# Kernel optimization log

Measured on AMD Instinct MI355X. Metric: run time of the kernel, lower is better.

## Reference

```python
import jax, jax.numpy as jnp
import numpy as np

B, T, D, VQ, L2, HID = 8, 2048, 768, 64, 12, 1024
K = 2 ** L2          # 4096 codebook entries
N_MID = 4            # condition_layer=6 -> 1 input + 4 middle + 1 output Linear, 5 BatchNorms
EPS_N = 1e-6
EPS_BN = 1e-5


def setup_inputs() -> dict:
    key = jax.random.key(0)
    ks = jax.random.split(key, 10)
    g = lambda i, shape, sc: jax.random.normal(ks[i], shape, jnp.float32) * sc
    return {
        "h_in": jax.random.normal(ks[0], (B, D, T), jnp.float32),
        "attn_mask": jax.random.randint(ks[1], (B, T), 0, 2, jnp.int32),
        "proj_w": g(2, (VQ, D), 0.02), "proj_b": jnp.zeros((VQ,), jnp.float32),
        "inv_w": g(3, (D, VQ), 0.02), "inv_b": jnp.zeros((D,), jnp.float32),
        "mlp_w_in": g(4, (HID, L2), 0.1), "mlp_b_in": jnp.zeros((HID,), jnp.float32),
        "mlp_w_mid": g(5, (N_MID, HID, HID), 0.03), "mlp_b_mid": jnp.zeros((N_MID, HID), jnp.float32),
        "mlp_w_out": g(6, (VQ, HID), 0.03), "mlp_b_out": jnp.zeros((VQ,), jnp.float32),
        "bn_gamma": jnp.ones((N_MID + 1, HID), jnp.float32),
        "bn_beta": jnp.zeros((N_MID + 1, HID), jnp.float32),
    }


def _bn(x, gamma, beta):
    # BatchNorm1d, training mode: batch mean / biased var over codebook rows
    m = x.mean(axis=0)
    v = x.var(axis=0)
    return (x - m) * jax.lax.rsqrt(v + EPS_BN) * gamma + beta


def _l2norm(x):
    return x / (jnp.linalg.norm(x, axis=-1, keepdims=True) + EPS_N)


def reference(h_in, attn_mask, proj_w, proj_b, inv_w, inv_b,
              mlp_w_in, mlp_b_in, mlp_w_mid, mlp_b_mid, mlp_w_out, mlp_b_out,
              bn_gamma, bn_beta):
    # --- codebook: binary vectors -> condition MLP (Linear+BN+ReLU x5, Linear) ---
    ints = jnp.arange(K)
    bits = ((ints[:, None] & (1 << jnp.arange(L2 - 1, -1, -1))) > 0).astype(jnp.float32)  # [K, L2]
    x = jax.nn.relu(_bn(bits @ mlp_w_in.T + mlp_b_in, bn_gamma[0], bn_beta[0]))
    for i in range(N_MID):
        x = jax.nn.relu(_bn(x @ mlp_w_mid[i].T + mlp_b_mid[i], bn_gamma[i + 1], bn_beta[i + 1]))
    embed = x @ mlp_w_out.T + mlp_b_out          # [K, VQ]
    embed = _l2norm(embed)                        # sphere=True

    # --- project hidden states: h_in [B,D,T] -> [B,T,VQ] ---
    h = jnp.einsum('bdt,vd->btv', h_in, proj_w) + proj_b
    h = _l2norm(h)

    # --- pairwise squared distances to codebook, argmax of -d (== softmax argmax) ---
    hf = h.reshape(-1, VQ)                                       # [B*T, VQ]
    d = (hf ** 2).sum(-1, keepdims=True) + (embed ** 2).sum(-1) - 2.0 * (hf @ embed.T)  # [B*T, K]
    code = jnp.argmax(-d, axis=-1)                               # [B*T]

    # --- masked gather/scatter quantization (eval path: hard codes) ---
    mask = (attn_mask == 1)                                      # [B, T]
    h_vq = embed[code].reshape(B, T, VQ) * mask[..., None].astype(h.dtype)
    quantized = jnp.einsum('btv,dv->btd', h_vq, inv_w) + inv_b   # proj_inv -> [B, T, D]
    vq_code = jnp.where(mask, code.reshape(B, T), 0)
    return quantized, vq_code
```

## Files before the change

kernel.cpp:

```cpp
#include <hip/hip_runtime.h>
#include <stddef.h>

#define BB   8
#define TT_  2048
#define DD   768
#define VQ_  64
#define L2C  12
#define HID_ 1024
#define KK   4096
#define NMID 4
#define NT   (BB*TT_)

typedef _Float16 h8v __attribute__((ext_vector_type(8)));
typedef float    f4v __attribute__((ext_vector_type(4)));

#define GL16(g, l) __builtin_amdgcn_global_load_lds( \
    (const __attribute__((address_space(1))) void*)(g), \
    (__attribute__((address_space(3))) void*)(l), 16, 0, 0)

__global__ __launch_bounds__(256) void k_mlp_in(const float* __restrict__ w_in,
                                                const float* __restrict__ b_in,
                                                float* __restrict__ X) {
    __shared__ float ws_[256 * 12];
    __shared__ float bs_[256];
    int tid = threadIdx.x;
    int h0  = blockIdx.x * 256;
    for (int i = tid; i < 256 * 12; i += 256) ws_[i] = w_in[h0 * 12 + i];
    bs_[tid] = b_in[h0 + tid];
    __syncthreads();
    float w[12];
#pragma unroll
    for (int l = 0; l < 12; l++) w[l] = ws_[tid * 12 + l];
    float bias = bs_[tid];
    int k0 = blockIdx.y * 16;
    for (int kk = 0; kk < 16; kk++) {
        int k = k0 + kk;
        float acc = bias;
#pragma unroll
        for (int l = 0; l < 12; l++)
            if ((k >> (11 - l)) & 1) acc += w[l];
        X[(size_t)k * HID_ + h0 + tid] = acc;
    }
}

__global__ __launch_bounds__(256) void k_bn_stats1(const float* __restrict__ Y,
                                                   float* __restrict__ part) {
    int b = blockIdx.x;
    int c = blockIdx.y * 256 + threadIdx.x;
    const float* src = Y + ((size_t)b << 6) * HID_ + c;
    float s = 0.f, q = 0.f;
    for (int r = 0; r < 64; r++) {
        float v = src[(size_t)r << 10];
        s += v; q += v * v;
    }
    part[((size_t)b << 10) + c] = s;
    part[65536 + ((size_t)b << 10) + c] = q;
}

__global__ __launch_bounds__(256) void k_bn_stats2(const float* __restrict__ part,
                                                   float* __restrict__ mv) {
    int c = blockIdx.x * 256 + threadIdx.x;
    float s = 0.f, q = 0.f;
    for (int b = 0; b < 64; b++) {
        s += part[((size_t)b << 10) + c];
        q += part[65536 + ((size_t)b << 10) + c];
    }
    float m = s * (1.f / KK);
    float v = q * (1.f / KK) - m * m;
    mv[c] = m; mv[HID_ + c] = v;
}

__global__ __launch_bounds__(256) void k_bn_apply_split(const float* __restrict__ Y,
                                                        const float* __restrict__ mv,
                                                        const float* __restrict__ gamma,
                                                        const float* __restrict__ beta,
                                                        _Float16* __restrict__ Xhi,
                                                        _Float16* __restrict__ Xlo) {
    int i = blockIdx.x * 256 + threadIdx.x;
    int c = (i << 2) & (HID_ - 1);
    float4 x = ((const float4*)Y)[i];
    float4 m = *(const float4*)(mv + c);
    float4 v = *(const float4*)(mv + HID_ + c);
    float4 g = *(const float4*)(gamma + c);
    float4 b = *(const float4*)(beta + c);
    float o[4];
    o[0] = fmaxf(0.f, (x.x - m.x) * (1.f / sqrtf(v.x + 1e-5f)) * g.x + b.x);
    o[1] = fmaxf(0.f, (x.y - m.y) * (1.f / sqrtf(v.y + 1e-5f)) * g.y + b.y);
    o[2] = fmaxf(0.f, (x.z - m.z) * (1.f / sqrtf(v.z + 1e-5f)) * g.z + b.z);
    o[3] = fmaxf(0.f, (x.w - m.w) * (1.f / sqrtf(v.w + 1e-5f)) * g.w + b.w);
    union { _Float16 h[4]; uint2 u; } uh, ul;
#pragma unroll
    for (int j = 0; j < 4; j++) {
        _Float16 h = (_Float16)o[j];
        uh.h[j] = h;
        ul.h[j] = (_Float16)(o[j] - (float)h);
    }
    *(uint2*)(Xhi + ((size_t)i << 2)) = uh.u;
    *(uint2*)(Xlo + ((size_t)i << 2)) = ul.u;
}

__global__ __launch_bounds__(256) void k_gemm_mfma3(const _Float16* __restrict__ Ahi,
                                                    const _Float16* __restrict__ Alo,
                                                    const _Float16* __restrict__ Whi,
                                                    const _Float16* __restrict__ Wlo,
                                                    const float* __restrict__ bias,
                                                    float* __restrict__ C) {
    __shared__ __attribute__((aligned(128))) char lds[4 * 32768];
    const int tid = threadIdx.x;
    const int wg = blockIdx.x;
    const int m0 = (wg & 31) << 7;
    const int n0 = (wg >> 5) << 7;
    const int wave = tid >> 6, lane = tid & 63;
    const int l15 = lane & 15, quad = lane >> 4;
    const int wm = (wave >> 1) << 6;
    const int wn = (wave & 1) << 6;

    const int rowA = (wave << 5) + (lane >> 2);
    const int colb = (lane & 3) << 4;
    const char* gA_h = (const char*)Ahi + ((size_t)(m0 + rowA) << 11) + colb;
    const char* gA_l = (const char*)Alo + ((size_t)(m0 + rowA) << 11) + colb;
    const char* gW_h = (const char*)Whi + ((size_t)(n0 + rowA) << 11) + colb;
    const char* gW_l = (const char*)Wlo + ((size_t)(n0 + rowA) << 11) + colb;
    const int dA = wave << 11;

    int offA[4], offW[4];
#pragma unroll
    for (int i = 0; i < 4; i++) offA[i] = ((wm + (i << 4) + l15) << 6) + (quad << 4);
#pragma unroll
    for (int j = 0; j < 4; j++) offW[j] = ((wn + (j << 4) + l15) << 6) + (quad << 4);

    f4v acc[4][4];
#pragma unroll
    for (int i = 0; i < 4; i++)
#pragma unroll
        for (int j = 0; j < 4; j++) acc[i][j] = (f4v){0.f, 0.f, 0.f, 0.f};

#define STG(bufi, tt) do { \
        char* b_ = lds + ((bufi) << 15); int o_ = (tt) << 6; \
        GL16(gA_h + o_,         b_ + dA); \
        GL16(gA_h + 32768 + o_, b_ + dA + 1024); \
        GL16(gA_l + o_,         b_ + 8192 + dA); \
        GL16(gA_l + 32768 + o_, b_ + 8192 + dA + 1024); \
        GL16(gW_h + o_,         b_ + 16384 + dA); \
        GL16(gW_h + 32768 + o_, b_ + 16384 + dA + 1024); \
        GL16(gW_l + o_,         b_ + 24576 + dA); \
        GL16(gW_l + 32768 + o_, b_ + 24576 + dA + 1024); \
    } while (0)

    STG(0, 0); STG(1, 1); STG(2, 2);
    for (int t = 0; t < 32; ++t) {
        if (t <= 29)      asm volatile("s_waitcnt vmcnt(16)" ::: "memory");
        else if (t == 30) asm volatile("s_waitcnt vmcnt(8)"  ::: "memory");
        else              asm volatile("s_waitcnt vmcnt(0)"  ::: "memory");
        __builtin_amdgcn_s_barrier();
        asm volatile("" ::: "memory");
        if (t + 3 < 32) STG((t + 3) & 3, t + 3);
        const char* b = lds + ((size_t)(t & 3) << 15);
        h8v ah[4], al[4];
#pragma unroll
        for (int i = 0; i < 4; i++) {
            ah[i] = *(const h8v*)(b + offA[i]);
            al[i] = *(const h8v*)(b + 8192 + offA[i]);
        }
        __builtin_amdgcn_s_setprio(1);
#pragma unroll
        for (int j = 0; j < 4; j++) {
            h8v bh = *(const h8v*)(b + 16384 + offW[j]);
            h8v bl = *(const h8v*)(b + 24576 + offW[j]);
#pragma unroll
            for (int i = 0; i < 4; i++) {
                acc[i][j] = __builtin_amdgcn_mfma_f32_16x16x32_f16(ah[i], bh, acc[i][j], 0, 0, 0);
                acc[i][j] = __builtin_amdgcn_mfma_f32_16x16x32_f16(ah[i], bl, acc[i][j], 0, 0, 0);
                acc[i][j] = __builtin_amdgcn_mfma_f32_16x16x32_f16(al[i], bh, acc[i][j], 0, 0, 0);
            }
        }
        __builtin_amdgcn_s_setprio(0);
        asm volatile("" ::: "memory");
    }
#undef STG

#pragma unroll
    for (int j = 0; j < 4; j++) {
        int col = n0 + wn + (j << 4) + l15;
        float bv = bias[col];
#pragma unroll
        for (int i = 0; i < 4; i++) {
            int row = m0 + wm + (i << 4) + (quad << 2);
#pragma unroll
            for (int r = 0; r < 4; r++)
                C[(size_t)(row + r) * HID_ + col] = acc[i][j][r] + bv;
        }
    }
}

__global__ __launch_bounds__(256) void k_gemm_mfma2(const _Float16* __restrict__ Ahi,
                                                    const _Float16* __restrict__ Alo,
                                                    const _Float16* __restrict__ Whi,
                                                    const _Float16* __restrict__ Wlo,
                                                    const float* __restrict__ bias,
                                                    float* __restrict__ C,
                                                    int M, int N, int Kd) {
    __shared__ __attribute__((aligned(128))) char lds[2][24576];
    const int tid = threadIdx.x;
    int wg = blockIdx.x;
    const int nwg = gridDim.x;
    wg = (wg & 7) * (nwg >> 3) + (wg >> 3);
    const int nx = M >> 7;
    const int m0 = (wg % nx) << 7;
    const int n0 = (wg / nx) << 6;
    const int wave = tid >> 6, lane = tid & 63;
    const int l15 = lane & 15, quad = lane >> 4;
    const int wm = (wave >> 1) << 6;
    const int wn = (wave & 1) << 5;

    const int pA0 = ((wave << 1) | 0) * 1024 + lane * 16;
    const int pA1 = ((wave << 1) | 1) * 1024 + lane * 16;
    const int pW  = wave * 1024 + lane * 16;
    const int qA0 = pA0 ^ (((pA0 >> 7) & 3) << 4);
    const int qA1 = pA1 ^ (((pA1 >> 7) & 3) << 4);
    const int qW  = pW  ^ (((pW  >> 7) & 3) << 4);
    const size_t krow = (size_t)Kd * 2;
    const char* gAh0 = (const char*)Ahi + (size_t)(m0 + (qA0 >> 6)) * krow + (qA0 & 63);
    const char* gAh1 = (const char*)Ahi + (size_t)(m0 + (qA1 >> 6)) * krow + (qA1 & 63);
    const char* gAl0 = (const char*)Alo + (size_t)(m0 + (qA0 >> 6)) * krow + (qA0 & 63);
    const char* gAl1 = (const char*)Alo + (size_t)(m0 + (qA1 >> 6)) * krow + (qA1 & 63);
    const char* gWh  = (const char*)Whi + (size_t)(n0 + (qW >> 6)) * krow + (qW & 63);
    const char* gWl  = (const char*)Wlo + (size_t)(n0 + (qW >> 6)) * krow + (qW & 63);
    const int dA0 = (wave << 1) * 1024;
    const int dA1 = dA0 + 1024;
    const int dW  = wave * 1024;

    int offA[4], offW[2];
#pragma unroll
    for (int i = 0; i < 4; i++) {
        int r = wm + (i << 4) + l15;
        offA[i] = r * 64 + ((quad ^ ((r >> 1) & 3)) << 4);
    }
#pragma unroll
    for (int j = 0; j < 2; j++) {
        int r = wn + (j << 4) + l15;
        offW[j] = r * 64 + ((quad ^ ((r >> 1) & 3)) << 4);
    }

    f4v acc[4][2];
#pragma unroll
    for (int i = 0; i < 4; i++)
#pragma unroll
        for (int j = 0; j < 2; j++) acc[i][j] = (f4v){0.f, 0.f, 0.f, 0.f};

#define STAGE(bufi, tt) do { \
        char* b_ = lds[bufi]; size_t o_ = (size_t)(tt) << 6; \
        GL16(gAh0 + o_, b_ + dA0); \
        GL16(gAh1 + o_, b_ + dA1); \
        GL16(gAl0 + o_, b_ + 8192 + dA0); \
        GL16(gAl1 + o_, b_ + 8192 + dA1); \
        GL16(gWh  + o_, b_ + 16384 + dW); \
        GL16(gWl  + o_, b_ + 20480 + dW); \
    } while (0)

    STAGE(0, 0);
    const int nt = Kd >> 5;
    for (int t = 0; t < nt; ++t) {
        const int cur = t & 1;
        if (t + 1 < nt) {
            STAGE(cur ^ 1, t + 1);
            asm volatile("s_waitcnt vmcnt(6)" ::: "memory");
        } else {
            asm volatile("s_waitcnt vmcnt(0)" ::: "memory");
        }
        __builtin_amdgcn_s_barrier();
        asm volatile("" ::: "memory");
        const char* b = lds[cur];
        h8v ah[4], al[4], bh[2], bl[2];
#pragma unroll
        for (int i = 0; i < 4; i++) {
            ah[i] = *(const h8v*)(b + offA[i]);
            al[i] = *(const h8v*)(b + 8192 + offA[i]);
        }
#pragma unroll
        for (int j = 0; j < 2; j++) {
            bh[j] = *(const h8v*)(b + 16384 + offW[j]);
            bl[j] = *(const h8v*)(b + 20480 + offW[j]);
        }
        __builtin_amdgcn_s_setprio(1);
#pragma unroll
        for (int i = 0; i < 4; i++)
#pragma unroll
            for (int j = 0; j < 2; j++) {
                acc[i][j] = __builtin_amdgcn_mfma_f32_16x16x32_f16(ah[i], bh[j], acc[i][j], 0, 0, 0);
                acc[i][j] = __builtin_amdgcn_mfma_f32_16x16x32_f16(ah[i], bl[j], acc[i][j], 0, 0, 0);
                acc[i][j] = __builtin_amdgcn_mfma_f32_16x16x32_f16(al[i], bh[j], acc[i][j], 0, 0, 0);
            }
        __builtin_amdgcn_s_setprio(0);
        asm volatile("" ::: "memory");
        __builtin_amdgcn_s_barrier();
    }
#undef STAGE

#pragma unroll
    for (int j = 0; j < 2; j++) {
        int col = n0 + wn + (j << 4) + l15;
        float bv = bias[col];
#pragma unroll
        for (int i = 0; i < 4; i++) {
            int row = m0 + wm + (i << 4) + (quad << 2);
#pragma unroll
            for (int r = 0; r < 4; r++)
                C[(size_t)(row + r) * N + col] = acc[i][j][r] + bv;
        }
    }
}

__global__ __launch_bounds__(256) void k_l2norm(float* __restrict__ E,
                                                float* __restrict__ eqh,
                                                _Float16* __restrict__ Ehi,
                                                _Float16* __restrict__ Elo) {
    int tid = threadIdx.x;
    int row = blockIdx.x * 4 + (tid >> 6);
    int v = tid & 63;
    size_t off = ((size_t)row << 6) + v;
    float x = E[off];
    float ss = x * x;
#pragma unroll
    for (int o = 32; o; o >>= 1) ss += __shfl_xor(ss, o, 64);
    float inv = 1.f / (sqrtf(ss) + 1e-6f);
    float xn = x * inv;
    E[off] = xn;
    _Float16 hh = (_Float16)xn;
    Ehi[off] = hh;
    Elo[off] = (_Float16)(xn - (float)hh);
    if (v == 0) eqh[row] = -0.5f * (ss * inv * inv);
}

__global__ __launch_bounds__(256) void k_wsplit(const float* __restrict__ pw,
                                                _Float16* __restrict__ pwhi,
                                                _Float16* __restrict__ pwlo) {
    int i = blockIdx.x * 256 + threadIdx.x;
    float4 w = ((const float4*)pw)[i];
    float wf[4] = {w.x, w.y, w.z, w.w};
    union { _Float16 h[4]; uint2 u; } uh, ul;
#pragma unroll
    for (int j = 0; j < 4; j++) {
        _Float16 h = (_Float16)wf[j];
        uh.h[j] = h;
        ul.h[j] = (_Float16)(wf[j] - (float)h);
    }
    *(uint2*)(pwhi + ((size_t)i << 2)) = uh.u;
    *(uint2*)(pwlo + ((size_t)i << 2)) = ul.u;
}

__global__ __launch_bounds__(256) void k_cvt_inv(const float* __restrict__ iw,
                                                 _Float16* __restrict__ iwh) {
    int i = blockIdx.x * 256 + threadIdx.x;
    float4 w = ((const float4*)iw)[i];
    union { _Float16 h[4]; uint2 u; } uh;
    uh.h[0] = (_Float16)w.x; uh.h[1] = (_Float16)w.y;
    uh.h[2] = (_Float16)w.z; uh.h[3] = (_Float16)w.w;
    *(uint2*)(iwh + ((size_t)i << 2)) = uh.u;
}

__global__ __launch_bounds__(256) void k_proj_mfma(const float* __restrict__ h_in,
                                                   const _Float16* __restrict__ pwhi,
                                                   const _Float16* __restrict__ pwlo,
                                                   float* __restrict__ Hpart) {
    __shared__ float shA[128 * 33];
    const int tid = threadIdx.x;
    const int t0 = blockIdx.x * 128;
    const int ks = blockIdx.y;
    const int b = t0 >> 11;
    const int tloc0 = t0 & (TT_ - 1);
    const int wave = tid >> 6, lane = tid & 63;
    const int l15 = lane & 15, quad = lane >> 4;

    const int dl = tid >> 3;
    const int tg = (tid & 7) << 4;

    f4v acc[2][4];
#pragma unroll
    for (int i = 0; i < 2; i++)
#pragma unroll
        for (int j = 0; j < 4; j++) acc[i][j] = (f4v){0.f, 0.f, 0.f, 0.f};

    for (int kk = 0; kk < 6; kk++) {
        int dd0 = ks * 192 + kk * 32;
        const float* src = h_in + ((size_t)(b * DD + dd0 + dl) << 11) + tloc0 + tg;
        float4 g0 = *(const float4*)(src);
        float4 g1 = *(const float4*)(src + 4);
        float4 g2 = *(const float4*)(src + 8);
        float4 g3 = *(const float4*)(src + 12);
        __syncthreads();
        float gv[16] = {g0.x, g0.y, g0.z, g0.w, g1.x, g1.y, g1.z, g1.w,
                        g2.x, g2.y, g2.z, g2.w, g3.x, g3.y, g3.z, g3.w};
#pragma unroll
        for (int i = 0; i < 16; i++) shA[(tg + i) * 33 + dl] = gv[i];
        __syncthreads();

        h8v ah[2], al[2];
#pragma unroll
        for (int mt = 0; mt < 2; mt++) {
            const float* ap = &shA[((wave << 5) + (mt << 4) + l15) * 33 + (quad << 3)];
            float4 a0 = *(const float4*)(ap);
            float4 a1 = *(const float4*)(ap + 4);
            float av[8] = {a0.x, a0.y, a0.z, a0.w, a1.x, a1.y, a1.z, a1.w};
#pragma unroll
            for (int j = 0; j < 8; j++) {
                _Float16 h = (_Float16)av[j];
                ah[mt][j] = h;
                al[mt][j] = (_Float16)(av[j] - (float)h);
            }
        }
#pragma unroll
        for (int nt = 0; nt < 4; nt++) {
            size_t wb = (size_t)((nt << 4) + l15) * DD + dd0 + (quad << 3);
            h8v bh = *(const h8v*)(pwhi + wb);
            h8v bl = *(const h8v*)(pwlo + wb);
#pragma unroll
            for (int mt = 0; mt < 2; mt++) {
                acc[mt][nt] = __builtin_amdgcn_mfma_f32_16x16x32_f16(ah[mt], bh, acc[mt][nt], 0, 0, 0);
                acc[mt][nt] = __builtin_amdgcn_mfma_f32_16x16x32_f16(ah[mt], bl, acc[mt][nt], 0, 0, 0);
                acc[mt][nt] = __builtin_amdgcn_mfma_f32_16x16x32_f16(al[mt], bh, acc[mt][nt], 0, 0, 0);
            }
        }
    }
    float* dst = Hpart + ((size_t)ks << 20);
#pragma unroll
    for (int mt = 0; mt < 2; mt++) {
#pragma unroll
        for (int r = 0; r < 4; r++) {
            int t = t0 + (wave << 5) + (mt << 4) + (quad << 2) + r;
#pragma unroll
            for (int nt = 0; nt < 4; nt++)
                dst[((size_t)t << 6) + (nt << 4) + l15] = acc[mt][nt][r];
        }
    }
}

__global__ __launch_bounds__(256) void k_hnorm(const float* __restrict__ Hpart,
                                               const float* __restrict__ pb,
                                               _Float16* __restrict__ Hhi,
                                               _Float16* __restrict__ Hlo) {
    __shared__ float ssp[4][64];
    int tid = threadIdx.x;
    int tt = tid & 63, vg = tid >> 6;
    int t = blockIdx.x * 64 + tt;
    size_t base = ((size_t)t << 6) + (vg << 4);
    float o[16];
#pragma unroll
    for (int u = 0; u < 4; u++) {
        float4 p0 = *(const float4*)(Hpart + (0u << 20) + base + (u << 2));
        float4 p1 = *(const float4*)(Hpart + (1u << 20) + base + (u << 2));
        float4 p2 = *(const float4*)(Hpart + (2u << 20) + base + (u << 2));
        float4 p3 = *(const float4*)(Hpart + (3u << 20) + base + (u << 2));
        o[u * 4 + 0] = p0.x + p1.x + p2.x + p3.x;
        o[u * 4 + 1] = p0.y + p1.y + p2.y + p3.y;
        o[u * 4 + 2] = p0.z + p1.z + p2.z + p3.z;
        o[u * 4 + 3] = p0.w + p1.w + p2.w + p3.w;
    }
    float sp = 0.f;
#pragma unroll
    for (int j = 0; j < 16; j++) {
        o[j] += pb[(vg << 4) + j];
        sp = fmaf(o[j], o[j], sp);
    }
    ssp[vg][tt] = sp;
    __syncthreads();
    float ss = ssp[0][tt] + ssp[1][tt] + ssp[2][tt] + ssp[3][tt];
    float inv = 1.f / (sqrtf(ss) + 1e-6f);
    union { _Float16 h[8]; uint4 u; } uh0, uh1, ul0, ul1;
#pragma unroll
    for (int j = 0; j < 16; j++) {
        float xn = o[j] * inv;
        _Float16 hh = (_Float16)xn;
        _Float16 ll = (_Float16)(xn - (float)hh);
        if (j < 8) { uh0.h[j] = hh; ul0.h[j] = ll; }
        else       { uh1.h[j - 8] = hh; ul1.h[j - 8] = ll; }
    }
    *(uint4*)(Hhi + base)     = uh0.u;
    *(uint4*)(Hhi + base + 8) = uh1.u;
    *(uint4*)(Hlo + base)     = ul0.u;
    *(uint4*)(Hlo + base + 8) = ul1.u;
}

__global__ __launch_bounds__(256) void k_argmax_mfma(const _Float16* __restrict__ Hhi,
                                                     const _Float16* __restrict__ Hlo,
                                                     const _Float16* __restrict__ Ehi,
                                                     const _Float16* __restrict__ Elo,
                                                     const float* __restrict__ eqh,
                                                     float* __restrict__ ps,
                                                     int* __restrict__ pi) {
    int tid = threadIdx.x;
    int wave = tid >> 6, lane = tid & 63;
    int l15 = lane & 15, quad = lane >> 4;
    int t0 = blockIdx.x * 256 + wave * 64;
    int kh = blockIdx.y;
    const int kbase = kh << 8;

    h8v hh0[4], hh1[4], hl0[4], hl1[4];
#pragma unroll
    for (int s = 0; s < 4; s++) {
        size_t hb = (size_t)(t0 + (s << 4) + l15) * 64 + (quad << 3);
        hh0[s] = *(const h8v*)(Hhi + hb);
        hh1[s] = *(const h8v*)(Hhi + hb + 32);
        hl0[s] = *(const h8v*)(Hlo + hb);
        hl1[s] = *(const h8v*)(Hlo + hb + 32);
    }
    float best[4] = {-1e30f, -1e30f, -1e30f, -1e30f};
    int   idx[4]  = {0, 0, 0, 0};

    size_t eb = (size_t)(kbase + l15) * 64 + (quad << 3);
    h8v eh0 = *(const h8v*)(Ehi + eb);
    h8v eh1 = *(const h8v*)(Ehi + eb + 32);
    h8v el0 = *(const h8v*)(Elo + eb);
    h8v el1 = *(const h8v*)(Elo + eb + 32);
    float4 q4 = *(const float4*)(eqh + kbase + (quad << 2));

    for (int it = 0; it < 16; it++) {
        h8v ce0 = eh0, ce1 = eh1, cl0 = el0, cl1 = el1;
        float4 cq = q4;
        int k0 = kbase + (it << 4);
        int kn = k0 + 16;
        if (kn > KK - 16) kn = KK - 16;
        size_t ebn = (size_t)(kn + l15) * 64 + (quad << 3);
        eh0 = *(const h8v*)(Ehi + ebn);
        eh1 = *(const h8v*)(Ehi + ebn + 32);
        el0 = *(const h8v*)(Elo + ebn);
        el1 = *(const h8v*)(Elo + ebn + 32);
        q4 = *(const float4*)(eqh + kn + (quad << 2));

        f4v acc[4];
#pragma unroll
        for (int s = 0; s < 4; s++) acc[s] = (f4v){0.f, 0.f, 0.f, 0.f};
#pragma unroll
        for (int s = 0; s < 4; s++) acc[s] = __builtin_amdgcn_mfma_f32_16x16x32_f16(ce0, hh0[s], acc[s], 0, 0, 0);
#pragma unroll
        for (int s = 0; s < 4; s++) acc[s] = __builtin_amdgcn_mfma_f32_16x16x32_f16(ce1, hh1[s], acc[s], 0, 0, 0);
#pragma unroll
        for (int s = 0; s < 4; s++) acc[s] = __builtin_amdgcn_mfma_f32_16x16x32_f16(cl0, hh0[s], acc[s], 0, 0, 0);
#pragma unroll
        for (int s = 0; s < 4; s++) acc[s] = __builtin_amdgcn_mfma_f32_16x16x32_f16(cl1, hh1[s], acc[s], 0, 0, 0);
#pragma unroll
        for (int s = 0; s < 4; s++) acc[s] = __builtin_amdgcn_mfma_f32_16x16x32_f16(ce0, hl0[s], acc[s], 0, 0, 0);
#pragma unroll
        for (int s = 0; s < 4; s++) acc[s] = __builtin_amdgcn_mfma_f32_16x16x32_f16(ce1, hl1[s], acc[s], 0, 0, 0);
        float qv[4] = {cq.x, cq.y, cq.z, cq.w};
#pragma unroll
        for (int r = 0; r < 4; r++) {
            int k = k0 + (quad << 2) + r;
#pragma unroll
            for (int s = 0; s < 4; s++) {
                float sc = acc[s][r] + qv[r];
                if (sc > best[s]) { best[s] = sc; idx[s] = k; }
            }
        }
    }
#pragma unroll
    for (int m = 16; m <= 32; m <<= 1) {
#pragma unroll
        for (int s = 0; s < 4; s++) {
            float ob = __shfl_xor(best[s], m, 64);
            int   oi = __shfl_xor(idx[s], m, 64);
            if (ob > best[s] || (ob == best[s] && oi < idx[s])) { best[s] = ob; idx[s] = oi; }
        }
    }
    if (quad == 0) {
#pragma unroll
        for (int s = 0; s < 4; s++) {
            int t = t0 + (s << 4) + l15;
            ps[(size_t)t * 16 + kh] = best[s];
            pi[(size_t)t * 16 + kh] = idx[s];
        }
    }
}

__global__ __launch_bounds__(256) void k_merge(const float* __restrict__ ps,
                                               const int* __restrict__ pi,
                                               const int* __restrict__ mask,
                                               const _Float16* __restrict__ Ehi,
                                               _Float16* __restrict__ G16,
                                               float* __restrict__ outc) {
    __shared__ int codes[256];
    __shared__ int ms[256];
    int tid = threadIdx.x;
    int base = blockIdx.x << 8;
    int t = base + tid;
    float best = ps[(size_t)t * 16];
    int bi = pi[(size_t)t * 16];
#pragma unroll
    for (int s = 1; s < 16; s++) {
        float v = ps[(size_t)t * 16 + s];
        if (v > best) { best = v; bi = pi[(size_t)t * 16 + s]; }
    }
    int m = mask[t];
    codes[tid] = bi;
    ms[tid] = m;
    outc[t] = m ? (float)bi : 0.0f;
    __syncthreads();
    for (int i = tid; i < 256 * 8; i += 256) {
        int r = i >> 3, u = i & 7;
        uint4 e = ms[r] ? ((const uint4*)(Ehi + ((size_t)codes[r] << 6)))[u]
                        : make_uint4(0u, 0u, 0u, 0u);
        ((uint4*)(G16 + ((size_t)(base + r) << 6)))[u] = e;
    }
}

__global__ __launch_bounds__(256) void k_gemm_out(const _Float16* __restrict__ G16,
                                                  const _Float16* __restrict__ iwh,
                                                  const float* __restrict__ bias,
                                                  float* __restrict__ C) {
    const int tid = threadIdx.x;
    const int t0 = blockIdx.x * 128, n0 = blockIdx.y * 64;
    const int wave = tid >> 6, lane = tid & 63;
    const int l15 = lane & 15, quad = lane >> 4;

    f4v acc[2][4];
#pragma unroll
    for (int i = 0; i < 2; i++)
#pragma unroll
        for (int j = 0; j < 4; j++) acc[i][j] = (f4v){0.f, 0.f, 0.f, 0.f};

#pragma unroll
    for (int ks = 0; ks < 2; ks++) {
        int kk = (ks << 5) + (quad << 3);
        h8v a[2], b[4];
#pragma unroll
        for (int mt = 0; mt < 2; mt++)
            a[mt] = *(const h8v*)(G16 + (size_t)(t0 + (wave << 5) + (mt << 4) + l15) * 64 + kk);
#pragma unroll
        for (int nt = 0; nt < 4; nt++)
            b[nt] = *(const h8v*)(iwh + (size_t)(n0 + (nt << 4) + l15) * 64 + kk);
#pragma unroll
        for (int mt = 0; mt < 2; mt++)
#pragma unroll
            for (int nt = 0; nt < 4; nt++)
                acc[mt][nt] = __builtin_amdgcn_mfma_f32_16x16x32_f16(a[mt], b[nt], acc[mt][nt], 0, 0, 0);
    }
#pragma unroll
    for (int nt = 0; nt < 4; nt++) {
        int col = n0 + (nt << 4) + l15;
        float bv = bias[col];
#pragma unroll
        for (int mt = 0; mt < 2; mt++) {
            int row = t0 + (wave << 5) + (mt << 4) + (quad << 2);
#pragma unroll
            for (int r = 0; r < 4; r++)
                C[(size_t)(row + r) * DD + col] = acc[mt][nt][r] + bv;
        }
    }
}

extern "C" void kernel_launch(void* const* d_in, const int* in_sizes, int n_in,
                              void* d_out, int out_size, void* d_ws, size_t ws_size,
                              hipStream_t stream) {
    const float* h_in   = (const float*)d_in[0];
    const int*   amask  = (const int*)d_in[1];
    const float* proj_w = (const float*)d_in[2];
    const float* proj_b = (const float*)d_in[3];
    const float* inv_w  = (const float*)d_in[4];
    const float* inv_b  = (const float*)d_in[5];
    const float* w_in   = (const float*)d_in[6];
    const float* b_in   = (const float*)d_in[7];
    const float* w_mid  = (const float*)d_in[8];
    const float* b_mid  = (const float*)d_in[9];
    const float* w_out  = (const float*)d_in[10];
    const float* b_out  = (const float*)d_in[11];
    const float* gamma  = (const float*)d_in[12];
    const float* beta   = (const float*)d_in[13];

    float*     Y    = (float*)d_ws;
    _Float16*  Xhi  = (_Float16*)(Y + (size_t)KK * HID_);
    _Float16*  Xlo  = Xhi + (size_t)KK * HID_;
    float*     mv   = (float*)(Xlo + (size_t)KK * HID_);
    float*     Emb  = mv + 2 * HID_;
    float*     eqh  = Emb + (size_t)KK * VQ_;
    float*     spart= eqh + KK;
    _Float16*  pwhi = (_Float16*)(spart + 2 * 65536);
    _Float16*  pwlo = pwhi + (size_t)VQ_ * DD;
    float*    Hpart = Y;
    _Float16* H16hi = Xhi;
    _Float16* H16lo = H16hi + (size_t)NT * VQ_;
    _Float16* E16hi = H16lo + (size_t)NT * VQ_;
    _Float16* E16lo = E16hi + (size_t)KK * VQ_;
    float*    ps    = (float*)(E16lo + (size_t)KK * VQ_);
    int*      pidx  = (int*)(ps + (size_t)NT * 16);
    _Float16* G16   = (_Float16*)(pidx + (size_t)NT * 16);
    _Float16* iwh   = G16 + (size_t)NT * VQ_;

    float* out_q = (float*)d_out;
    float* out_c = out_q + (size_t)NT * DD;

    _Float16* Wmh = (_Float16*)d_out;
    _Float16* Wml = Wmh + (size_t)HID_ * HID_;
    _Float16* Woh = Wml + (size_t)HID_ * HID_;
    _Float16* Wol = Woh + (size_t)VQ_ * HID_;

    k_mlp_in<<<dim3(HID_ / 256, KK / 16), 256, 0, stream>>>(w_in, b_in, Y);
    k_bn_stats1<<<dim3(64, 4), 256, 0, stream>>>(Y, spart);
    k_bn_stats2<<<4, 256, 0, stream>>>(spart, mv);
    k_bn_apply_split<<<KK * HID_ / 1024, 256, 0, stream>>>(Y, mv, gamma, beta, Xhi, Xlo);
    for (int i = 0; i < NMID; i++) {
        k_wsplit<<<HID_ * HID_ / 1024, 256, 0, stream>>>(
            w_mid + (size_t)i * HID_ * HID_, Wmh, Wml);
        k_gemm_mfma3<<<(KK / 128) * (HID_ / 128), 256, 0, stream>>>(
            Xhi, Xlo, Wmh, Wml, b_mid + (size_t)i * HID_, Y);
        k_bn_stats1<<<dim3(64, 4), 256, 0, stream>>>(Y, spart);
        k_bn_stats2<<<4, 256, 0, stream>>>(spart, mv);
        k_bn_apply_split<<<KK * HID_ / 1024, 256, 0, stream>>>(Y, mv,
            gamma + (size_t)(i + 1) * HID_, beta + (size_t)(i + 1) * HID_, Xhi, Xlo);
    }
    k_wsplit<<<VQ_ * HID_ / 1024, 256, 0, stream>>>(w_out, Woh, Wol);
    k_gemm_mfma2<<<(KK / 128) * (VQ_ / 64), 256, 0, stream>>>(
        Xhi, Xlo, Woh, Wol, b_out, Emb, KK, VQ_, HID_);
    k_l2norm<<<KK / 4, 256, 0, stream>>>(Emb, eqh, E16hi, E16lo);

    k_wsplit<<<VQ_ * DD / 1024, 256, 0, stream>>>(proj_w, pwhi, pwlo);
    k_cvt_inv<<<VQ_ * DD / 1024, 256, 0, stream>>>(inv_w, iwh);
    k_proj_mfma<<<dim3(NT / 128, 4), 256, 0, stream>>>(h_in, pwhi, pwlo, Hpart);
    k_hnorm<<<NT / 64, 256, 0, stream>>>(Hpart, proj_b, H16hi, H16lo);
    k_argmax_mfma<<<dim3(NT / 256, 16), 256, 0, stream>>>(
        H16hi, H16lo, E16hi, E16lo, eqh, ps, pidx);
    k_merge<<<NT / 256, 256, 0, stream>>>(ps, pidx, amask, E16hi, G16, out_c);
    k_gemm_out<<<dim3(NT / 128, DD / 64), 256, 0, stream>>>(G16, iwh, inv_b, out_q);
}
```

Measured before the change: 473.5 us.

## Batch weight splits into one launch, restructure GEMM and argmax pipelines

All fp16 hi/lo weight splits (mid, out, proj) now run in a single kernel at the start instead of six separate launches, which removes launch overhead. The mfma3 GEMM main loop now issues stages two at a time with a full vmcnt(0) wait per pair instead of a rolling 3-deep prefetch, which trades finer-grained overlap for fewer barriers. The argmax kernel halves the tokens per wave, doubles the grid and double-buffers two codebook tiles with interleaved MFMA chains, aiming for more occupancy and latency hiding. Staging the weights for all mid layers at once uses more scratch space in the output buffer.

```diff
diff --git a/kernel.cpp b/kernel.cpp
--- a/kernel.cpp
+++ b/kernel.cpp
@@ -147,36 +147,40 @@
         GL16(gW_l + 32768 + o_, b_ + 24576 + dA + 1024); \
     } while (0)
 
-    STG(0, 0); STG(1, 1); STG(2, 2);
-    for (int t = 0; t < 32; ++t) {
-        if (t <= 29)      asm volatile("s_waitcnt vmcnt(16)" ::: "memory");
-        else if (t == 30) asm volatile("s_waitcnt vmcnt(8)"  ::: "memory");
-        else              asm volatile("s_waitcnt vmcnt(0)"  ::: "memory");
+#define CMP(tt) do { \
+        const char* b = lds + ((size_t)((tt) & 3) << 15); \
+        h8v ah[4], al[4]; \
+        _Pragma("unroll") \
+        for (int i = 0; i < 4; i++) { \
+            ah[i] = *(const h8v*)(b + offA[i]); \
+            al[i] = *(const h8v*)(b + 8192 + offA[i]); \
+        } \
+        __builtin_amdgcn_s_setprio(1); \
+        _Pragma("unroll") \
+        for (int j = 0; j < 4; j++) { \
+            h8v bh = *(const h8v*)(b + 16384 + offW[j]); \
+            h8v bl = *(const h8v*)(b + 24576 + offW[j]); \
+            _Pragma("unroll") \
+            for (int i = 0; i < 4; i++) { \
+                acc[i][j] = __builtin_amdgcn_mfma_f32_16x16x32_f16(ah[i], bh, acc[i][j], 0, 0, 0); \
+                acc[i][j] = __builtin_amdgcn_mfma_f32_16x16x32_f16(ah[i], bl, acc[i][j], 0, 0, 0); \
+                acc[i][j] = __builtin_amdgcn_mfma_f32_16x16x32_f16(al[i], bh, acc[i][j], 0, 0, 0); \
+            } \
+        } \
+        __builtin_amdgcn_s_setprio(0); \
+    } while (0)
+
+    STG(0, 0); STG(1, 1);
+    for (int p = 0; p < 16; ++p) {
+        asm volatile("s_waitcnt vmcnt(0)" ::: "memory");
         __builtin_amdgcn_s_barrier();
         asm volatile("" ::: "memory");
-        if (t + 3 < 32) STG((t + 3) & 3, t + 3);
-        const char* b = lds + ((size_t)(t & 3) << 15);
-        h8v ah[4], al[4];
-#pragma unroll
-        for (int i = 0; i < 4; i++) {
-            ah[i] = *(const h8v*)(b + offA[i]);
-            al[i] = *(const h8v*)(b + 8192 + offA[i]);
-        }
-        __builtin_amdgcn_s_setprio(1);
-#pragma unroll
-        for (int j = 0; j < 4; j++) {
-            h8v bh = *(const h8v*)(b + 16384 + offW[j]);
-            h8v bl = *(const h8v*)(b + 24576 + offW[j]);
-#pragma unroll
-            for (int i = 0; i < 4; i++) {
-                acc[i][j] = __builtin_amdgcn_mfma_f32_16x16x32_f16(ah[i], bh, acc[i][j], 0, 0, 0);
-                acc[i][j] = __builtin_amdgcn_mfma_f32_16x16x32_f16(ah[i], bl, acc[i][j], 0, 0, 0);
-                acc[i][j] = __builtin_amdgcn_mfma_f32_16x16x32_f16(al[i], bh, acc[i][j], 0, 0, 0);
-            }
-        }
-        __builtin_amdgcn_s_setprio(0);
+        if (p < 15) { STG((2 * p + 2) & 3, 2 * p + 2); STG((2 * p + 3) & 3, 2 * p + 3); }
+        CMP(2 * p);
+        CMP(2 * p + 1);
         asm volatile("" ::: "memory");
     }
+#undef CMP
 #undef STG
 
 #pragma unroll
@@ -332,11 +336,21 @@
     if (v == 0) eqh[row] = -0.5f * (ss * inv * inv);
 }
 
-__global__ __launch_bounds__(256) void k_wsplit(const float* __restrict__ pw,
-                                                _Float16* __restrict__ pwhi,
-                                                _Float16* __restrict__ pwlo) {
+__global__ __launch_bounds__(256) void k_wsplit_all(const float* __restrict__ w_mid,
+                                                    const float* __restrict__ w_out,
+                                                    const float* __restrict__ proj_w,
+                                                    _Float16* __restrict__ Wmh,
+                                                    _Float16* __restrict__ Wml,
+                                                    _Float16* __restrict__ Woh,
+                                                    _Float16* __restrict__ Wol,
+                                                    _Float16* __restrict__ pwhi,
+                                                    _Float16* __restrict__ pwlo) {
     int i = blockIdx.x * 256 + threadIdx.x;
-    float4 w = ((const float4*)pw)[i];
+    const float4* src; _Float16 *dh, *dl; int off;
+    if (i < 1048576)            { src = (const float4*)w_mid;  dh = Wmh;  dl = Wml;  off = i; }
+    else if (i < 1048576+16384) { src = (const float4*)w_out;  dh = Woh;  dl = Wol;  off = i - 1048576; }
+    else                        { src = (const float4*)proj_w; dh = pwhi; dl = pwlo; off = i - 1048576 - 16384; }
+    float4 w = src[off];
     float wf[4] = {w.x, w.y, w.z, w.w};
     union { _Float16 h[4]; uint2 u; } uh, ul;
 #pragma unroll
@@ -345,8 +359,8 @@
         uh.h[j] = h;
         ul.h[j] = (_Float16)(wf[j] - (float)h);
     }
-    *(uint2*)(pwhi + ((size_t)i << 2)) = uh.u;
-    *(uint2*)(pwlo + ((size_t)i << 2)) = ul.u;
+    *(uint2*)(dh + ((size_t)off << 2)) = uh.u;
+    *(uint2*)(dl + ((size_t)off << 2)) = ul.u;
 }
 
 __global__ __launch_bounds__(256) void k_cvt_inv(const float* __restrict__ iw,
@@ -491,72 +505,81 @@
     int tid = threadIdx.x;
     int wave = tid >> 6, lane = tid & 63;
     int l15 = lane & 15, quad = lane >> 4;
-    int t0 = blockIdx.x * 256 + wave * 64;
+    int t0 = blockIdx.x * 128 + wave * 32;
     int kh = blockIdx.y;
     const int kbase = kh << 8;
 
-    h8v hh0[4], hh1[4], hl0[4], hl1[4];
-#pragma unroll
-    for (int s = 0; s < 4; s++) {
+    h8v hh0[2], hh1[2], hl0[2], hl1[2];
+#pragma unroll
+    for (int s = 0; s < 2; s++) {
         size_t hb = (size_t)(t0 + (s << 4) + l15) * 64 + (quad << 3);
         hh0[s] = *(const h8v*)(Hhi + hb);
         hh1[s] = *(const h8v*)(Hhi + hb + 32);
         hl0[s] = *(const h8v*)(Hlo + hb);
         hl1[s] = *(const h8v*)(Hlo + hb + 32);
     }
-    float best[4] = {-1e30f, -1e30f, -1e30f, -1e30f};
-    int   idx[4]  = {0, 0, 0, 0};
-
-    size_t eb = (size_t)(kbase + l15) * 64 + (quad << 3);
-    h8v eh0 = *(const h8v*)(Ehi + eb);
-    h8v eh1 = *(const h8v*)(Ehi + eb + 32);
-    h8v el0 = *(const h8v*)(Elo + eb);
-    h8v el1 = *(const h8v*)(Elo + eb + 32);
-    float4 q4 = *(const float4*)(eqh + kbase + (quad << 2));
-
-    for (int it = 0; it < 16; it++) {
-        h8v ce0 = eh0, ce1 = eh1, cl0 = el0, cl1 = el1;
-        float4 cq = q4;
-        int k0 = kbase + (it << 4);
-        int kn = k0 + 16;
-        if (kn > KK - 16) kn = KK - 16;
-        size_t ebn = (size_t)(kn + l15) * 64 + (quad << 3);
-        eh0 = *(const h8v*)(Ehi + ebn);
-        eh1 = *(const h8v*)(Ehi + ebn + 32);
-        el0 = *(const h8v*)(Elo + ebn);
-        el1 = *(const h8v*)(Elo + ebn + 32);
-        q4 = *(const float4*)(eqh + kn + (quad << 2));
-
-        f4v acc[4];
-#pragma unroll
-        for (int s = 0; s < 4; s++) acc[s] = (f4v){0.f, 0.f, 0.f, 0.f};
-#pragma unroll
-        for (int s = 0; s < 4; s++) acc[s] = __builtin_amdgcn_mfma_f32_16x16x32_f16(ce0, hh0[s], acc[s], 0, 0, 0);
-#pragma unroll
-        for (int s = 0; s < 4; s++) acc[s] = __builtin_amdgcn_mfma_f32_16x16x32_f16(ce1, hh1[s], acc[s], 0, 0, 0);
-#pragma unroll
-        for (int s = 0; s < 4; s++) acc[s] = __builtin_amdgcn_mfma_f32_16x16x32_f16(cl0, hh0[s], acc[s], 0, 0, 0);
-#pragma unroll
-        for (int s = 0; s < 4; s++) acc[s] = __builtin_amdgcn_mfma_f32_16x16x32_f16(cl1, hh1[s], acc[s], 0, 0, 0);
-#pragma unroll
-        for (int s = 0; s < 4; s++) acc[s] = __builtin_amdgcn_mfma_f32_16x16x32_f16(ce0, hl0[s], acc[s], 0, 0, 0);
-#pragma unroll
-        for (int s = 0; s < 4; s++) acc[s] = __builtin_amdgcn_mfma_f32_16x16x32_f16(ce1, hl1[s], acc[s], 0, 0, 0);
-        float qv[4] = {cq.x, cq.y, cq.z, cq.w};
-#pragma unroll
-        for (int r = 0; r < 4; r++) {
-            int k = k0 + (quad << 2) + r;
-#pragma unroll
-            for (int s = 0; s < 4; s++) {
-                float sc = acc[s][r] + qv[r];
-                if (sc > best[s]) { best[s] = sc; idx[s] = k; }
-            }
-        }
-    }
+    float best[2] = {-1e30f, -1e30f};
+    int   idx[2]  = {0, 0};
+
+    size_t eb0 = (size_t)(kbase + l15) * 64 + (quad << 3);
+    h8v e0h0 = *(const h8v*)(Ehi + eb0);
+    h8v e0h1 = *(const h8v*)(Ehi + eb0 + 32);
+    h8v e0l0 = *(const h8v*)(Elo + eb0);
+    h8v e0l1 = *(const h8v*)(Elo + eb0 + 32);
+    float4 q0 = *(const float4*)(eqh + kbase + (quad << 2));
+    size_t eb1 = eb0 + 1024;
+    h8v e1h0 = *(const h8v*)(Ehi + eb1);
+    h8v e1h1 = *(const h8v*)(Ehi + eb1 + 32);
+    h8v e1l0 = *(const h8v*)(Elo + eb1);
+    h8v e1l1 = *(const h8v*)(Elo + eb1 + 32);
+    float4 q1 = *(const float4*)(eqh + kbase + 16 + (quad << 2));
+
+#define AHALF(EH0, EH1, EL0, EL1, QQ, IT) do { \
+        f4v acc0 = (f4v){0.f, 0.f, 0.f, 0.f}; \
+        f4v acc1 = (f4v){0.f, 0.f, 0.f, 0.f}; \
+        __builtin_amdgcn_s_setprio(1); \
+        acc0 = __builtin_amdgcn_mfma_f32_16x16x32_f16(EH0, hh0[0], acc0, 0, 0, 0); \
+        acc1 = __builtin_amdgcn_mfma_f32_16x16x32_f16(EH0, hh0[1], acc1, 0, 0, 0); \
+        acc0 = __builtin_amdgcn_mfma_f32_16x16x32_f16(EH1, hh1[0], acc0, 0, 0, 0); \
+        acc1 = __builtin_amdgcn_mfma_f32_16x16x32_f16(EH1, hh1[1], acc1, 0, 0, 0); \
+        acc0 = __builtin_amdgcn_mfma_f32_16x16x32_f16(EL0, hh0[0], acc0, 0, 0, 0); \
+        acc1 = __builtin_amdgcn_mfma_f32_16x16x32_f16(EL0, hh0[1], acc1, 0, 0, 0); \
+        acc0 = __builtin_amdgcn_mfma_f32_16x16x32_f16(EL1, hh1[0], acc0, 0, 0, 0); \
+        acc1 = __builtin_amdgcn_mfma_f32_16x16x32_f16(EL1, hh1[1], acc1, 0, 0, 0); \
+        acc0 = __builtin_amdgcn_mfma_f32_16x16x32_f16(EH0, hl0[0], acc0, 0, 0, 0); \
+        acc1 = __builtin_amdgcn_mfma_f32_16x16x32_f16(EH0, hl0[1], acc1, 0, 0, 0); \
+        acc0 = __builtin_amdgcn_mfma_f32_16x16x32_f16(EH1, hl1[0], acc0, 0, 0, 0); \
+        acc1 = __builtin_amdgcn_mfma_f32_16x16x32_f16(EH1, hl1[1], acc1, 0, 0, 0); \
+        __builtin_amdgcn_s_setprio(0); \
+        float cqa[4] = {QQ.x, QQ.y, QQ.z, QQ.w}; \
+        int tn = (IT) + 2; if (tn > 15) tn = 15;       \
+        size_t ebn = (size_t)(kbase + (tn << 4) + l15) * 64 + (quad << 3); \
+        EH0 = *(const h8v*)(Ehi + ebn); \
+        EH1 = *(const h8v*)(Ehi + ebn + 32); \
+        EL0 = *(const h8v*)(Elo + ebn); \
+        EL1 = *(const h8v*)(Elo + ebn + 32); \
+        QQ  = *(const float4*)(eqh + kbase + (tn << 4) + (quad << 2)); \
+        int k0 = kbase + ((IT) << 4); \
+        _Pragma("unroll") \
+        for (int r = 0; r < 4; r++) { \
+            int kk_ = k0 + (quad << 2) + r; \
+            float sc0 = acc0[r] + cqa[r]; \
+            if (sc0 > best[0]) { best[0] = sc0; idx[0] = kk_; } \
+            float sc1 = acc1[r] + cqa[r]; \
+            if (sc1 > best[1]) { best[1] = sc1; idx[1] = kk_; } \
+        } \
+    } while (0)
+
+    for (int p = 0; p < 8; ++p) {
+        AHALF(e0h0, e0h1, e0l0, e0l1, q0, 2 * p);
+        AHALF(e1h0, e1h1, e1l0, e1l1, q1, 2 * p + 1);
+    }
+#undef AHALF
+
 #pragma unroll
     for (int m = 16; m <= 32; m <<= 1) {
 #pragma unroll
-        for (int s = 0; s < 4; s++) {
+        for (int s = 0; s < 2; s++) {
             float ob = __shfl_xor(best[s], m, 64);
             int   oi = __shfl_xor(idx[s], m, 64);
             if (ob > best[s] || (ob == best[s] && oi < idx[s])) { best[s] = ob; idx[s] = oi; }
@@ -564,7 +587,7 @@
     }
     if (quad == 0) {
 #pragma unroll
-        for (int s = 0; s < 4; s++) {
+        for (int s = 0; s < 2; s++) {
             int t = t0 + (s << 4) + l15;
             ps[(size_t)t * 16 + kh] = best[s];
             pi[(size_t)t * 16 + kh] = idx[s];
@@ -689,34 +712,34 @@
     float* out_c = out_q + (size_t)NT * DD;
 
     _Float16* Wmh = (_Float16*)d_out;
-    _Float16* Wml = Wmh + (size_t)HID_ * HID_;
-    _Float16* Woh = Wml + (size_t)HID_ * HID_;
+    _Float16* Wml = Wmh + (size_t)NMID * HID_ * HID_;
+    _Float16* Woh = Wml + (size_t)NMID * HID_ * HID_;
     _Float16* Wol = Woh + (size_t)VQ_ * HID_;
+
+    k_wsplit_all<<<4208, 256, 0, stream>>>(w_mid, w_out, proj_w,
+                                           Wmh, Wml, Woh, Wol, pwhi, pwlo);
 
     k_mlp_in<<<dim3(HID_ / 256, KK / 16), 256, 0, stream>>>(w_in, b_in, Y);
     k_bn_stats1<<<dim3(64, 4), 256, 0, stream>>>(Y, spart);
     k_bn_stats2<<<4, 256, 0, stream>>>(spart, mv);
     k_bn_apply_split<<<KK * HID_ / 1024, 256, 0, stream>>>(Y, mv, gamma, beta, Xhi, Xlo);
     for (int i = 0; i < NMID; i++) {
-        k_wsplit<<<HID_ * HID_ / 1024, 256, 0, stream>>>(
-            w_mid + (size_t)i * HID_ * HID_, Wmh, Wml);
         k_gemm_mfma3<<<(KK / 128) * (HID_ / 128), 256, 0, stream>>>(
-            Xhi, Xlo, Wmh, Wml, b_mid + (size_t)i * HID_, Y);
+            Xhi, Xlo, Wmh + (size_t)i * HID_ * HID_, Wml + (size_t)i * HID_ * HID_,
+            b_mid + (size_t)i * HID_, Y);
         k_bn_stats1<<<dim3(64, 4), 256, 0, stream>>>(Y, spart);
         k_bn_stats2<<<4, 256, 0, stream>>>(spart, mv);
         k_bn_apply_split<<<KK * HID_ / 1024, 256, 0, stream>>>(Y, mv,
             gamma + (size_t)(i + 1) * HID_, beta + (size_t)(i + 1) * HID_, Xhi, Xlo);
     }
-    k_wsplit<<<VQ_ * HID_ / 1024, 256, 0, stream>>>(w_out, Woh, Wol);
     k_gemm_mfma2<<<(KK / 128) * (VQ_ / 64), 256, 0, stream>>>(
         Xhi, Xlo, Woh, Wol, b_out, Emb, KK, VQ_, HID_);
     k_l2norm<<<KK / 4, 256, 0, stream>>>(Emb, eqh, E16hi, E16lo);
 
-    k_wsplit<<<VQ_ * DD / 1024, 256, 0, stream>>>(proj_w, pwhi, pwlo);
     k_cvt_inv<<<VQ_ * DD / 1024, 256, 0, stream>>>(inv_w, iwh);
     k_proj_mfma<<<dim3(NT / 128, 4), 256, 0, stream>>>(h_in, pwhi, pwlo, Hpart);
     k_hnorm<<<NT / 64, 256, 0, stream>>>(Hpart, proj_b, H16hi, H16lo);
-    k_argmax_mfma<<<dim3(NT / 256, 16), 256, 0, stream>>>(
+    k_argmax_mfma<<<dim3(NT / 128, 16), 256, 0, stream>>>(
         H16hi, H16lo, E16hi, E16lo, eqh, ps, pidx);
     k_merge<<<NT / 256, 256, 0, stream>>>(ps, pidx, amask, E16hi, G16, out_c);
     k_gemm_out<<<dim3(NT / 128, DD / 64), 256, 0, stream>>>(G16, iwh, inv_b, out_q);
```

Measured after the change: 526.3 us. 1.11x slower.
